# Kernel tuning notes

Hardware: AMD Instinct MI355X
Metric: run time of the kernel (lower is better)

Reference implementation:

```python
import jax, jax.numpy as jnp
import numpy as np

B, S, D, H = 2, 2048, 1024, 16
HID = 1024  # hidden_dim

def setup_inputs() -> dict:
    key = jax.random.key(0)
    ks = jax.random.split(key, 9)
    sc = 1.0 / np.sqrt(D)
    return {
        "x": jax.random.normal(ks[0], (B, S, D), dtype=jnp.float32),
        "Wq": jax.random.normal(ks[1], (HID, D), dtype=jnp.float32) * sc,
        "bq": jnp.zeros((HID,), dtype=jnp.float32),
        "Wk": jax.random.normal(ks[2], (HID, D), dtype=jnp.float32) * sc,
        "bk": jnp.zeros((HID,), dtype=jnp.float32),
        "Wv": jax.random.normal(ks[3], (HID, D), dtype=jnp.float32) * sc,
        "bv": jnp.zeros((HID,), dtype=jnp.float32),
        "Wo": jax.random.normal(ks[4], (D, HID), dtype=jnp.float32) * (1.0 / np.sqrt(HID)),
        "bo": jnp.zeros((D,), dtype=jnp.float32),
    }

def reference(x, Wq, bq, Wk, bk, Wv, bv, Wo, bo):
    num_heads = H
    hd = HID // num_heads
    q = x @ Wq.T + bq  # [B,S,HID]
    k = x @ Wk.T + bk
    v = x @ Wv.T + bv
    # [B,S,H,hd] -> [B,H,S,hd]
    q = q.reshape(B, S, num_heads, hd).transpose(0, 2, 1, 3)
    k = k.reshape(B, S, num_heads, hd).transpose(0, 2, 1, 3)
    v = v.reshape(B, S, num_heads, hd).transpose(0, 2, 1, 3)
    # NOTE: original scales by sqrt(hidden_dim), not sqrt(head_dim)
    scores = jnp.einsum('bhqd,bhkd->bhqk', q, k) / jnp.sqrt(jnp.float32(HID))
    attn = jax.nn.softmax(scores, axis=-1)
    out = jnp.einsum('bhqk,bhkd->bhqd', attn, v)  # [B,H,S,hd]
    out = out.transpose(0, 2, 1, 3).reshape(B, S, HID)
    return out @ Wo.T + bo
```

## Files before the change

kernel.cpp:

```cpp
#include <hip/hip_runtime.h>
#include <hip/hip_bf16.h>


typedef __bf16 bf16;
typedef bf16 bf16x8 __attribute__((ext_vector_type(8)));
typedef float f32x4 __attribute__((ext_vector_type(4)));

#define MFMA16(Af, Bf, Cf) __builtin_amdgcn_mfma_f32_16x16x32_bf16((Af), (Bf), (Cf), 0, 0, 0)

__device__ __forceinline__ void gl_lds16(const void* g, void* l) {
    __builtin_amdgcn_global_load_lds(
        (const __attribute__((address_space(1))) void*)g,
        (__attribute__((address_space(3))) void*)l, 16, 0, 0);
}

__device__ __forceinline__ float exp2_fast(float x) {
    float r; asm("v_exp_f32 %0, %1" : "=v"(r) : "v"(x)); return r;
}

__global__ __launch_bounds__(256) void cvt_all(
    const float* __restrict__ x, const float* __restrict__ Wq,
    const float* __restrict__ Wk, const float* __restrict__ Wv,
    const float* __restrict__ Wo,
    bf16* __restrict__ xb, bf16* __restrict__ wqb, bf16* __restrict__ wkb,
    bf16* __restrict__ wvb, bf16* __restrict__ wob)
{
    const size_t i8 = ((size_t)blockIdx.x * 256 + threadIdx.x) * 8;
    const float* src; bf16* dst; size_t off;
    if (i8 < 4194304)      { src = x;  dst = xb;  off = i8; }
    else if (i8 < 5242880) { src = Wq; dst = wqb; off = i8 - 4194304; }
    else if (i8 < 6291456) { src = Wk; dst = wkb; off = i8 - 5242880; }
    else if (i8 < 7340032) { src = Wv; dst = wvb; off = i8 - 6291456; }
    else                   { src = Wo; dst = wob; off = i8 - 7340032; }
    f32x4 a = *reinterpret_cast<const f32x4*>(src + off);
    f32x4 b = *reinterpret_cast<const f32x4*>(src + off + 4);
    bf16x8 o;
    o[0]=(bf16)a[0]; o[1]=(bf16)a[1]; o[2]=(bf16)a[2]; o[3]=(bf16)a[3];
    o[4]=(bf16)b[0]; o[5]=(bf16)b[1]; o[6]=(bf16)b[2]; o[7]=(bf16)b[3];
    *reinterpret_cast<bf16x8*>(dst + off) = o;
}

__global__ __launch_bounds__(512) void qkv_gemm(
    const bf16* __restrict__ xb,
    const bf16* __restrict__ wqb, const bf16* __restrict__ wkb,
    const bf16* __restrict__ wvb,
    const float* __restrict__ bq, const float* __restrict__ bk,
    const float* __restrict__ bv,
    bf16* __restrict__ qo, bf16* __restrict__ ko, bf16* __restrict__ vo)
{
    __shared__ __align__(16) char smem[65536];

    const int which = blockIdx.y;
    const bf16* W     = (which == 0) ? wqb : (which == 1) ? wkb : wvb;
    const float* bia  = (which == 0) ? bq : (which == 1) ? bk : bv;
    bf16* outp        = (which == 0) ? qo : (which == 1) ? ko : vo;
    const float scale = (which == 0) ? 0.04508422f : 1.0f;

    const int bid0 = blockIdx.x;
    const int xcd = bid0 & 7, j = bid0 >> 3;
    const int tm = xcd * 4 + (j & 3);
    const int tn = j >> 2;
    const int m0 = tm * 128, n0 = tn * 128;

    const int t = threadIdx.x;
    const int l = t & 63, w = t >> 6;
    const int wr = w >> 1, wc = w & 1;
    const int lg = l >> 4, lr = l & 15;

    f32x4 acc[2][4];
#pragma unroll
    for (int i = 0; i < 2; ++i)
#pragma unroll
        for (int jj = 0; jj < 4; ++jj)
            acc[i][jj] = (f32x4){0.f, 0.f, 0.f, 0.f};

    auto stage = [&](int kt, char* base) {
        char* AsB = base;
        char* BsB = base + 16384;
#pragma unroll
        for (int i = 0; i < 2; ++i) {
            const int c = w * 128 + i * 64 + l;
            const int row = c >> 3, cc = (c & 7) ^ (row & 7);
            gl_lds16(xb + (size_t)(m0 + row) * 1024 + kt + cc * 8, AsB + c * 16);
            gl_lds16(W  + (size_t)(n0 + row) * 1024 + kt + cc * 8, BsB + c * 16);
        }
    };

    stage(0, smem);
    __syncthreads();

    for (int it = 0; it < 16; ++it) {
        char* base = smem + ((it & 1) << 15);
        if (it < 15) stage((it + 1) * 64, smem + (((it + 1) & 1) << 15));
        char* AsB = base;
        char* BsB = base + 16384;

#pragma unroll
        for (int ks = 0; ks < 2; ++ks) {
            bf16x8 af[2], bff[4];
#pragma unroll
            for (int i = 0; i < 2; ++i) {
                const int ar = wr * 32 + i * 16 + lr;
                af[i]  = *reinterpret_cast<bf16x8*>(AsB + ar * 128 + ((ks * 64 + (lg << 4)) ^ ((ar & 7) << 4)));
            }
#pragma unroll
            for (int i = 0; i < 4; ++i) {
                const int br = wc * 64 + i * 16 + lr;
                bff[i] = *reinterpret_cast<bf16x8*>(BsB + br * 128 + ((ks * 64 + (lg << 4)) ^ ((br & 7) << 4)));
            }
            if (which == 2) {
#pragma unroll
                for (int mi = 0; mi < 2; ++mi)
#pragma unroll
                    for (int ni = 0; ni < 4; ++ni)
                        acc[mi][ni] = MFMA16(bff[ni], af[mi], acc[mi][ni]);
            } else {
#pragma unroll
                for (int mi = 0; mi < 2; ++mi)
#pragma unroll
                    for (int ni = 0; ni < 4; ++ni)
                        acc[mi][ni] = MFMA16(af[mi], bff[ni], acc[mi][ni]);
            }
        }
        __syncthreads();
    }

    if (which == 2) {
#pragma unroll
        for (int ni = 0; ni < 4; ++ni) {
#pragma unroll
            for (int mi = 0; mi < 2; ++mi) {
#pragma unroll
                for (int r = 0; r < 4; ++r) {
                    const int col = n0 + wc * 64 + ni * 16 + lg * 4 + r;
                    const int h = col >> 6, d = col & 63;
                    const int rowg = m0 + wr * 32 + mi * 16 + lr;
                    const int b = rowg >> 11, s = rowg & 2047;
                    const int key = s & 127;
                    const int pos = (key & 96) | ((key & 12) << 1) | ((key & 16) >> 2) | (key & 3);
                    const float v = acc[mi][ni][r] + bia[col];
                    outp[((size_t)(b * 16 + h) * 64 + d) * 2048 + (s & ~127) + pos] = (bf16)v;
                }
            }
        }
    } else {
#pragma unroll
        for (int ni = 0; ni < 4; ++ni) {
            const int col = n0 + wc * 64 + ni * 16 + lr;
            const float bval = bia[col];
            const int h = col >> 6, d = col & 63;
#pragma unroll
            for (int mi = 0; mi < 2; ++mi) {
#pragma unroll
                for (int r = 0; r < 4; ++r) {
                    const int rowg = m0 + wr * 32 + mi * 16 + lg * 4 + r;
                    const int b = rowg >> 11, s = rowg & 2047;
                    const float v = (acc[mi][ni][r] + bval) * scale;
                    outp[((size_t)(b * 16 + h) * 2048 + s) * 64 + d] = (bf16)v;
                }
            }
        }
    }
}

__global__ __launch_bounds__(512, 4) void attn_kernel(
    const bf16* __restrict__ qb, const bf16* __restrict__ kb,
    const bf16* __restrict__ vb, bf16* __restrict__ ao)
{
    __shared__ __align__(16) char smem[65536];

    const int bid0 = blockIdx.x;
    const int bid = ((bid0 & 7) << 6) | (bid0 >> 3);
    const int qt = bid & 15, bh = bid >> 4;
    const int b = bh >> 4, h = bh & 15;
    const bf16* qp = qb + ((size_t)bh * 2048 + qt * 128) * 64;
    const bf16* kp = kb + (size_t)bh * 2048 * 64;
    const bf16* vt = vb + (size_t)bh * 64 * 2048;

    const int t = threadIdx.x;
    const int l = t & 63, w = t >> 6;
    const int g = w >> 2, ws = w & 3;
    const int lg = l >> 4, lr = l & 15;

    bf16x8 qf[2][2];
#pragma unroll
    for (int mt = 0; mt < 2; ++mt)
#pragma unroll
        for (int ks = 0; ks < 2; ++ks)
            qf[mt][ks] = *reinterpret_cast<const bf16x8*>(
                qp + (ws * 32 + mt * 16 + lr) * 64 + ks * 32 + lg * 8);

    f32x4 oacc[2][4];
#pragma unroll
    for (int mt = 0; mt < 2; ++mt)
#pragma unroll
        for (int jj = 0; jj < 4; ++jj)
            oacc[mt][jj] = (f32x4){0.f, 0.f, 0.f, 0.f};
    f32x4 lacc[2];
    lacc[0] = (f32x4){0.f, 0.f, 0.f, 0.f};
    lacc[1] = (f32x4){0.f, 0.f, 0.f, 0.f};

    bf16x8 vone;
#pragma unroll
    for (int jj = 0; jj < 8; ++jj) vone[jj] = (bf16)1.0f;

    auto stageKV = [&](int it, char* base) {
        const int kt = g * 16 + it;
        const bf16* ksrc = kp + (size_t)kt * 4096;
        char* KsB = base + g * 8192;
        char* VtB = base + 16384 + g * 8192;
#pragma unroll
        for (int i = 0; i < 2; ++i) {
            const int c = ws * 128 + i * 64 + l;
            const int row = c >> 3, cc = (c & 7) ^ (row & 7);
            gl_lds16(ksrc + (size_t)row * 64 + cc * 8, KsB + c * 16);
        }
#pragma unroll
        for (int i = 0; i < 2; ++i) {
            const int c = ws * 128 + i * 64 + l;
            const int d = c >> 3, i16 = c & 7;
            gl_lds16(vt + (size_t)d * 2048 + kt * 64 + ((i16 ^ (d & 7)) << 3),
                     VtB + c * 16);
        }
    };

    stageKV(0, smem);
    __syncthreads();

    for (int it = 0; it < 16; ++it) {
        char* base = smem + ((it & 1) << 15);
        if (it < 15) stageKV(it + 1, smem + (((it + 1) & 1) << 15));

        char* KsB = base + g * 8192;
        char* VtB = base + 16384 + g * 8192;

        f32x4 sc[2][4];
        __builtin_amdgcn_s_setprio(1);
#pragma unroll
        for (int nt = 0; nt < 4; ++nt) {
            sc[0][nt] = (f32x4){0.f, 0.f, 0.f, 0.f};
            sc[1][nt] = (f32x4){0.f, 0.f, 0.f, 0.f};
#pragma unroll
            for (int ks = 0; ks < 2; ++ks) {
                const int nrow = nt * 16 + lr;
                bf16x8 kf = *reinterpret_cast<bf16x8*>(
                    KsB + nrow * 128 + ((ks * 64 + (lg << 4)) ^ ((nrow & 7) << 4)));
                sc[0][nt] = MFMA16(kf, qf[0][ks], sc[0][nt]);
                sc[1][nt] = MFMA16(kf, qf[1][ks], sc[1][nt]);
            }
        }
        __builtin_amdgcn_s_setprio(0);

        bf16x8 pa[2][2];
#pragma unroll
        for (int mt = 0; mt < 2; ++mt)
#pragma unroll
            for (int k4 = 0; k4 < 2; ++k4)
#pragma unroll
                for (int jj = 0; jj < 8; ++jj)
                    pa[mt][k4][jj] = (bf16)exp2_fast(sc[mt][2 * k4 + (jj >> 2)][jj & 3]);

        __builtin_amdgcn_s_setprio(1);
#pragma unroll
        for (int k4 = 0; k4 < 2; ++k4) {
            lacc[0] = MFMA16(pa[0][k4], vone, lacc[0]);
            lacc[1] = MFMA16(pa[1][k4], vone, lacc[1]);
#pragma unroll
            for (int dt = 0; dt < 4; ++dt) {
                const int d = dt * 16 + lr;
                bf16x8 vf = *reinterpret_cast<bf16x8*>(
                    VtB + d * 128 + (((k4 << 6) + (lg << 4)) ^ ((d & 7) << 4)));
                oacc[0][dt] = MFMA16(pa[0][k4], vf, oacc[0][dt]);
                oacc[1][dt] = MFMA16(pa[1][k4], vf, oacc[1][dt]);
            }
        }
        __builtin_amdgcn_s_setprio(0);

        __syncthreads();
    }

    float* cb = (float*)smem;
    const int base = (ws * 64 + l) * 21;
#pragma unroll
    for (int mt = 0; mt < 2; ++mt) {
        if (g == 1) {
#pragma unroll
            for (int dt = 0; dt < 4; ++dt)
#pragma unroll
                for (int r = 0; r < 4; ++r)
                    cb[base + dt * 4 + r] = oacc[mt][dt][r];
#pragma unroll
            for (int r = 0; r < 4; ++r)
                cb[base + 16 + r] = lacc[mt][r];
        }
        __syncthreads();
        if (g == 0) {
#pragma unroll
            for (int dt = 0; dt < 4; ++dt)
#pragma unroll
                for (int r = 0; r < 4; ++r)
                    oacc[mt][dt][r] += cb[base + dt * 4 + r];
#pragma unroll
            for (int r = 0; r < 4; ++r)
                lacc[mt][r] += cb[base + 16 + r];
        }
        __syncthreads();
    }

    if (g == 0) {
#pragma unroll
        for (int mt = 0; mt < 2; ++mt) {
            float rl[4];
#pragma unroll
            for (int r = 0; r < 4; ++r) rl[r] = 1.0f / lacc[mt][r];
#pragma unroll
            for (int dt = 0; dt < 4; ++dt) {
#pragma unroll
                for (int r = 0; r < 4; ++r) {
                    const int qrow = qt * 128 + ws * 32 + mt * 16 + lg * 4 + r;
                    const int col = h * 64 + dt * 16 + lr;
                    ao[((size_t)b * 2048 + qrow) * 1024 + col] = (bf16)(oacc[mt][dt][r] * rl[r]);
                }
            }
        }
    }
}

__global__ __launch_bounds__(512) void out_gemm(
    const bf16* __restrict__ A, const bf16* __restrict__ Wb,
    const float* __restrict__ bo, float* __restrict__ out)
{
    __shared__ __align__(16) char smem[49152];

    const int bid0 = blockIdx.x;
    const int xcd = bid0 & 7, j = bid0 >> 3;
    const int tm = xcd * 4 + (j & 3);
    const int tn = j >> 2;
    const int m0 = tm * 128, n0 = tn * 64;

    const int t = threadIdx.x;
    const int l = t & 63, w = t >> 6;
    const int wr = w >> 1, wc = w & 1;
    const int lg = l >> 4, lr = l & 15;

    f32x4 acc[2][2];
#pragma unroll
    for (int i = 0; i < 2; ++i)
#pragma unroll
        for (int jj = 0; jj < 2; ++jj)
            acc[i][jj] = (f32x4){0.f, 0.f, 0.f, 0.f};

    auto stage = [&](int kt, char* base) {
        char* AsB = base;
        char* BsB = base + 16384;
#pragma unroll
        for (int i = 0; i < 2; ++i) {
            const int c = w * 128 + i * 64 + l;
            const int row = c >> 3, cc = (c & 7) ^ (row & 7);
            gl_lds16(A + (size_t)(m0 + row) * 1024 + kt + cc * 8, AsB + c * 16);
        }
        {
            const int c = w * 64 + l;
            const int row = c >> 3, cc = (c & 7) ^ (row & 7);
            gl_lds16(Wb + (size_t)(n0 + row) * 1024 + kt + cc * 8, BsB + c * 16);
        }
    };

    stage(0, smem);
    __syncthreads();

    for (int it = 0; it < 16; ++it) {
        char* base = smem + (it & 1) * 24576;
        if (it < 15) stage((it + 1) * 64, smem + ((it + 1) & 1) * 24576);
        char* AsB = base;
        char* BsB = base + 16384;

#pragma unroll
        for (int ks = 0; ks < 2; ++ks) {
            bf16x8 af[2], bff[2];
#pragma unroll
            for (int i = 0; i < 2; ++i) {
                const int ar = wr * 32 + i * 16 + lr;
                af[i] = *reinterpret_cast<bf16x8*>(AsB + ar * 128 + ((ks * 64 + (lg << 4)) ^ ((ar & 7) << 4)));
            }
#pragma unroll
            for (int i = 0; i < 2; ++i) {
                const int br = wc * 32 + i * 16 + lr;
                bff[i] = *reinterpret_cast<bf16x8*>(BsB + br * 128 + ((ks * 64 + (lg << 4)) ^ ((br & 7) << 4)));
            }
#pragma unroll
            for (int mi = 0; mi < 2; ++mi)
#pragma unroll
                for (int ni = 0; ni < 2; ++ni)
                    acc[mi][ni] = MFMA16(af[mi], bff[ni], acc[mi][ni]);
        }
        __syncthreads();
    }

#pragma unroll
    for (int ni = 0; ni < 2; ++ni) {
        const int col = n0 + wc * 32 + ni * 16 + lr;
        const float bval = bo[col];
#pragma unroll
        for (int mi = 0; mi < 2; ++mi) {
#pragma unroll
            for (int r = 0; r < 4; ++r) {
                const int rowg = m0 + wr * 32 + mi * 16 + lg * 4 + r;
                out[(size_t)rowg * 1024 + col] = acc[mi][ni][r] + bval;
            }
        }
    }
}

extern "C" void kernel_launch(void* const* d_in, const int* in_sizes, int n_in,
                              void* d_out, int out_size, void* d_ws, size_t ws_size,
                              hipStream_t stream) {
    (void)in_sizes; (void)n_in; (void)out_size; (void)ws_size;
    const float* x  = (const float*)d_in[0];
    const float* Wq = (const float*)d_in[1];
    const float* bq = (const float*)d_in[2];
    const float* Wk = (const float*)d_in[3];
    const float* bk = (const float*)d_in[4];
    const float* Wv = (const float*)d_in[5];
    const float* bv = (const float*)d_in[6];
    const float* Wo = (const float*)d_in[7];
    const float* bo = (const float*)d_in[8];
    float* out = (float*)d_out;

    bf16* xb   = (bf16*)d_ws;
    bf16* wqb  = xb   + 4194304;
    bf16* wkb  = wqb  + 1048576;
    bf16* wvb  = wkb  + 1048576;
    bf16* wob  = wvb  + 1048576;
    bf16* qbuf = wob  + 1048576;
    bf16* kbuf = qbuf + 4194304;
    bf16* vbuf = kbuf + 4194304;
    bf16* aob  = vbuf + 4194304;

    cvt_all<<<4096, 256, 0, stream>>>(x, Wq, Wk, Wv, Wo, xb, wqb, wkb, wvb, wob);
    qkv_gemm<<<dim3(256, 3), 512, 0, stream>>>(xb, wqb, wkb, wvb, bq, bk, bv, qbuf, kbuf, vbuf);
    attn_kernel<<<512, 512, 0, stream>>>(qbuf, kbuf, vbuf, aob);
    out_gemm<<<512, 512, 0, stream>>>(aob, wob, bo, out);
}
```

Baseline: 88.79 us.

## Software-pipeline attention: overlap PV of previous tile with QK and exp of current

The attention loop is restructured so the P·V MFMA step for the previous key tile runs after the current QK^T, before the current tile's exp. V gets a triple-buffered LDS ring so the previous tile's V stays resident while the next is staged. The aim is to interleave exp (VALU/transcendental) work with MFMA work across iterations and hide latency. LDS grows from 64KB to 80KB per block, which can cut how many blocks fit per CU under the launch bounds of 4.

```diff
diff --git a/kernel.cpp b/kernel.cpp
--- a/kernel.cpp
+++ b/kernel.cpp
@@ -167,7 +167,7 @@
     const bf16* __restrict__ qb, const bf16* __restrict__ kb,
     const bf16* __restrict__ vb, bf16* __restrict__ ao)
 {
-    __shared__ __align__(16) char smem[65536];
+    __shared__ __align__(16) char smem[81920];
 
     const int bid0 = blockIdx.x;
     const int bid = ((bid0 & 7) << 6) | (bid0 >> 3);
@@ -204,17 +204,20 @@
 #pragma unroll
     for (int jj = 0; jj < 8; ++jj) vone[jj] = (bf16)1.0f;
 
-    auto stageKV = [&](int it, char* base) {
+    auto stageK = [&](int it) {
         const int kt = g * 16 + it;
         const bf16* ksrc = kp + (size_t)kt * 4096;
-        char* KsB = base + g * 8192;
-        char* VtB = base + 16384 + g * 8192;
+        char* KsB = smem + ((it & 1) << 14) + g * 8192;
 #pragma unroll
         for (int i = 0; i < 2; ++i) {
             const int c = ws * 128 + i * 64 + l;
             const int row = c >> 3, cc = (c & 7) ^ (row & 7);
             gl_lds16(ksrc + (size_t)row * 64 + cc * 8, KsB + c * 16);
         }
+    };
+    auto stageV = [&](int it, int vbuf) {
+        const int kt = g * 16 + it;
+        char* VtB = smem + 32768 + (vbuf << 14) + g * 8192;
 #pragma unroll
         for (int i = 0; i < 2; ++i) {
             const int c = ws * 128 + i * 64 + l;
@@ -224,16 +227,32 @@
         }
     };
 
-    stageKV(0, smem);
+    bf16x8 pa[2][2];
+
+    auto pvStep = [&](char* VtB) {
+#pragma unroll
+        for (int k4 = 0; k4 < 2; ++k4) {
+            lacc[0] = MFMA16(pa[0][k4], vone, lacc[0]);
+            lacc[1] = MFMA16(pa[1][k4], vone, lacc[1]);
+#pragma unroll
+            for (int dt = 0; dt < 4; ++dt) {
+                const int d = dt * 16 + lr;
+                bf16x8 vf = *reinterpret_cast<bf16x8*>(
+                    VtB + d * 128 + (((k4 << 6) + (lg << 4)) ^ ((d & 7) << 4)));
+                oacc[0][dt] = MFMA16(pa[0][k4], vf, oacc[0][dt]);
+                oacc[1][dt] = MFMA16(pa[1][k4], vf, oacc[1][dt]);
+            }
+        }
+    };
+
+    stageK(0); stageV(0, 0);
     __syncthreads();
 
+    int vcur = 0, vnext = 1, vprev = 2;
     for (int it = 0; it < 16; ++it) {
-        char* base = smem + ((it & 1) << 15);
-        if (it < 15) stageKV(it + 1, smem + (((it + 1) & 1) << 15));
-
-        char* KsB = base + g * 8192;
-        char* VtB = base + 16384 + g * 8192;
-
+        if (it < 15) { stageK(it + 1); stageV(it + 1, vnext); }
+
+        char* KsB = smem + ((it & 1) << 14) + g * 8192;
         f32x4 sc[2][4];
         __builtin_amdgcn_s_setprio(1);
 #pragma unroll
@@ -251,7 +270,13 @@
         }
         __builtin_amdgcn_s_setprio(0);
 
-        bf16x8 pa[2][2];
+        if (it > 0) {
+            char* VtB = smem + 32768 + (vprev << 14) + g * 8192;
+            __builtin_amdgcn_s_setprio(1);
+            pvStep(VtB);
+            __builtin_amdgcn_s_setprio(0);
+        }
+
 #pragma unroll
         for (int mt = 0; mt < 2; ++mt)
 #pragma unroll
@@ -260,27 +285,18 @@
                 for (int jj = 0; jj < 8; ++jj)
                     pa[mt][k4][jj] = (bf16)exp2_fast(sc[mt][2 * k4 + (jj >> 2)][jj & 3]);
 
-        __builtin_amdgcn_s_setprio(1);
-#pragma unroll
-        for (int k4 = 0; k4 < 2; ++k4) {
-            lacc[0] = MFMA16(pa[0][k4], vone, lacc[0]);
-            lacc[1] = MFMA16(pa[1][k4], vone, lacc[1]);
-#pragma unroll
-            for (int dt = 0; dt < 4; ++dt) {
-                const int d = dt * 16 + lr;
-                bf16x8 vf = *reinterpret_cast<bf16x8*>(
-                    VtB + d * 128 + (((k4 << 6) + (lg << 4)) ^ ((d & 7) << 4)));
-                oacc[0][dt] = MFMA16(pa[0][k4], vf, oacc[0][dt]);
-                oacc[1][dt] = MFMA16(pa[1][k4], vf, oacc[1][dt]);
-            }
-        }
-        __builtin_amdgcn_s_setprio(0);
-
         __syncthreads();
+        const int tmp = vprev; vprev = vcur; vcur = vnext; vnext = tmp;
+    }
+
+    {
+        char* VtB = smem + 32768 + (vprev << 14) + g * 8192;
+        pvStep(VtB);
     }
 
     float* cb = (float*)smem;
     const int base = (ws * 64 + l) * 21;
+    __syncthreads();
 #pragma unroll
     for (int mt = 0; mt < 2; ++mt) {
         if (g == 1) {
```

Result: slower. 91.33 us (+2.9%).

## Drop split-KV wave groups in attention, use single 4-wave group over all keys

Applied to the files above, without the earlier changes.

The attention kernel previously split the key range across two 4-wave groups per block and merged their partial outputs through shared memory at the end. Now each block has 256 threads that walk all 32 key tiles, with half the LDS and no cross-group reduction. This removes the LDS merge and its barriers and allows more blocks per CU. In exchange each block has a serial loop twice as long and less intra-block parallelism for latency hiding.

```diff
diff --git a/kernel.cpp b/kernel.cpp
--- a/kernel.cpp
+++ b/kernel.cpp
@@ -163,11 +163,11 @@
     }
 }
 
-__global__ __launch_bounds__(512, 4) void attn_kernel(
+__global__ __launch_bounds__(256, 5) void attn_kernel(
     const bf16* __restrict__ qb, const bf16* __restrict__ kb,
     const bf16* __restrict__ vb, bf16* __restrict__ ao)
 {
-    __shared__ __align__(16) char smem[65536];
+    __shared__ __align__(16) char smem[32768];
 
     const int bid0 = blockIdx.x;
     const int bid = ((bid0 & 7) << 6) | (bid0 >> 3);
@@ -178,8 +178,7 @@
     const bf16* vt = vb + (size_t)bh * 64 * 2048;
 
     const int t = threadIdx.x;
-    const int l = t & 63, w = t >> 6;
-    const int g = w >> 2, ws = w & 3;
+    const int l = t & 63, ws = t >> 6;
     const int lg = l >> 4, lr = l & 15;
 
     bf16x8 qf[2][2];
@@ -204,11 +203,10 @@
 #pragma unroll
     for (int jj = 0; jj < 8; ++jj) vone[jj] = (bf16)1.0f;
 
-    auto stageKV = [&](int it, char* base) {
-        const int kt = g * 16 + it;
+    auto stageKV = [&](int kt, char* base) {
         const bf16* ksrc = kp + (size_t)kt * 4096;
-        char* KsB = base + g * 8192;
-        char* VtB = base + 16384 + g * 8192;
+        char* KsB = base;
+        char* VtB = base + 8192;
 #pragma unroll
         for (int i = 0; i < 2; ++i) {
             const int c = ws * 128 + i * 64 + l;
@@ -227,12 +225,12 @@
     stageKV(0, smem);
     __syncthreads();
 
-    for (int it = 0; it < 16; ++it) {
-        char* base = smem + ((it & 1) << 15);
-        if (it < 15) stageKV(it + 1, smem + (((it + 1) & 1) << 15));
-
-        char* KsB = base + g * 8192;
-        char* VtB = base + 16384 + g * 8192;
+    for (int it = 0; it < 32; ++it) {
+        char* base = smem + ((it & 1) << 14);
+        if (it < 31) stageKV(it + 1, smem + (((it + 1) & 1) << 14));
+
+        char* KsB = base;
+        char* VtB = base + 8192;
 
         f32x4 sc[2][4];
         __builtin_amdgcn_s_setprio(1);
@@ -279,48 +277,18 @@
         __syncthreads();
     }
 
-    float* cb = (float*)smem;
-    const int base = (ws * 64 + l) * 21;
 #pragma unroll
     for (int mt = 0; mt < 2; ++mt) {
-        if (g == 1) {
-#pragma unroll
-            for (int dt = 0; dt < 4; ++dt)
-#pragma unroll
-                for (int r = 0; r < 4; ++r)
-                    cb[base + dt * 4 + r] = oacc[mt][dt][r];
-#pragma unroll
-            for (int r = 0; r < 4; ++r)
-                cb[base + 16 + r] = lacc[mt][r];
-        }
-        __syncthreads();
-        if (g == 0) {
-#pragma unroll
-            for (int dt = 0; dt < 4; ++dt)
-#pragma unroll
-                for (int r = 0; r < 4; ++r)
-                    oacc[mt][dt][r] += cb[base + dt * 4 + r];
-#pragma unroll
-            for (int r = 0; r < 4; ++r)
-                lacc[mt][r] += cb[base + 16 + r];
-        }
-        __syncthreads();
-    }
-
-    if (g == 0) {
-#pragma unroll
-        for (int mt = 0; mt < 2; ++mt) {
-            float rl[4];
-#pragma unroll
-            for (int r = 0; r < 4; ++r) rl[r] = 1.0f / lacc[mt][r];
-#pragma unroll
-            for (int dt = 0; dt < 4; ++dt) {
-#pragma unroll
-                for (int r = 0; r < 4; ++r) {
-                    const int qrow = qt * 128 + ws * 32 + mt * 16 + lg * 4 + r;
-                    const int col = h * 64 + dt * 16 + lr;
-                    ao[((size_t)b * 2048 + qrow) * 1024 + col] = (bf16)(oacc[mt][dt][r] * rl[r]);
-                }
+        float rl[4];
+#pragma unroll
+        for (int r = 0; r < 4; ++r) rl[r] = 1.0f / lacc[mt][r];
+#pragma unroll
+        for (int dt = 0; dt < 4; ++dt) {
+#pragma unroll
+            for (int r = 0; r < 4; ++r) {
+                const int qrow = qt * 128 + ws * 32 + mt * 16 + lg * 4 + r;
+                const int col = h * 64 + dt * 16 + lr;
+                ao[((size_t)b * 2048 + qrow) * 1024 + col] = (bf16)(oacc[mt][dt][r] * rl[r]);
             }
         }
     }
@@ -439,6 +407,6 @@
 
     cvt_all<<<4096, 256, 0, stream>>>(x, Wq, Wk, Wv, Wo, xb, wqb, wkb, wvb, wob);
     qkv_gemm<<<dim3(256, 3), 512, 0, stream>>>(xb, wqb, wkb, wvb, bq, bk, bv, qbuf, kbuf, vbuf);
-    attn_kernel<<<512, 512, 0, stream>>>(qbuf, kbuf, vbuf, aob);
+    attn_kernel<<<512, 256, 0, stream>>>(qbuf, kbuf, vbuf, aob);
     out_gemm<<<512, 512, 0, stream>>>(aob, wob, bo, out);
 }
```

After: 140.5 us. 1.58x slower.
